# Performance work log

Measured on AMD Instinct MI355X. Metric: run time of the kernel, lower is better.

## Reference

```python
import jax, jax.numpy as jnp
import numpy as np

B, S, I, W, H = 32, 2048, 32, 20, 128  # batch, seq_len, input_size, window_size, hidden_size
LN_EPS = 1e-5


def setup_inputs() -> dict:
    key = jax.random.key(0)
    ks = jax.random.split(key, 12)
    sc = lambda fan: 1.0 / np.sqrt(fan)
    x = jax.random.normal(ks[0], (B, S, I), jnp.float32)
    # encoder: Linear(W*I -> H) + LayerNorm(H) (+ GELU, dropout inactive at eval)
    W_enc = jax.random.normal(ks[1], (W * I, H), jnp.float32) * sc(W * I)
    b_enc = jnp.zeros((H,), jnp.float32)
    gamma = jnp.ones((H,), jnp.float32)
    beta = jnp.zeros((H,), jnp.float32)
    # comparator: Linear(2H->H), GELU, Linear(H->H//2), GELU, Linear(H//2->1), Sigmoid
    W1 = jax.random.normal(ks[2], (2 * H, H), jnp.float32) * sc(2 * H)
    b1 = jnp.zeros((H,), jnp.float32)
    W2 = jax.random.normal(ks[3], (H, H // 2), jnp.float32) * sc(H)
    b2 = jnp.zeros((H // 2,), jnp.float32)
    W3 = jax.random.normal(ks[4], (H // 2, 1), jnp.float32) * sc(H // 2)
    b3 = jnp.zeros((1,), jnp.float32)
    return dict(x=x, W_enc=W_enc, b_enc=b_enc, gamma=gamma, beta=beta,
                W1=W1, b1=b1, W2=W2, b2=b2, W3=W3, b3=b3)


def _gelu(v):
    return jax.nn.gelu(v, approximate=False)  # torch nn.GELU default is exact erf


def reference(x, W_enc, b_enc, gamma, beta, W1, b1, W2, b2, W3, b3):
    Bs, Ss, Is = x.shape
    Wd = W_enc.shape[0] // Is  # window_size
    nwin = Ss - Wd + 1
    # gather all sliding windows once: (B, nwin, Wd*I)
    idx = jnp.arange(nwin)[:, None] + jnp.arange(Wd)[None, :]
    win = x[:, idx, :].reshape(Bs, nwin, Wd * Is)
    # encoder: one big GEMM over all windows (before(t) == window at t-Wd, after(t) == window at t)
    h = win @ W_enc + b_enc
    mu = jnp.mean(h, axis=-1, keepdims=True)
    var = jnp.mean((h - mu) ** 2, axis=-1, keepdims=True)
    enc = _gelu((h - mu) / jnp.sqrt(var + LN_EPS) * gamma + beta)  # (B, nwin, H)
    T = Ss - 2 * Wd  # number of valid changepoint positions t in [Wd, Ss-Wd)
    combined = jnp.concatenate([enc[:, :T], enc[:, Wd:Wd + T]], axis=-1)  # (B, T, 2H)
    z = _gelu(combined @ W1 + b1)
    z = _gelu(z @ W2 + b2)
    p = jax.nn.sigmoid((z @ W3 + b3)[..., 0])  # (B, T)
    probs = jnp.pad(p, ((0, 0), (Wd, Wd)))  # zero pad to (B, S)
    return probs, probs > 0.5
```

## Files before the change

kernel.cpp:

```cpp
#include <hip/hip_runtime.h>
#include <hip/hip_bf16.h>
#include <math.h>

namespace {

constexpr int kB = 32;
constexpr int kS = 2048;
constexpr int kI = 32;
constexpr int kW = 20;
constexpr int kH = 128;
constexpr int kNwin = kS - kW + 1;
constexpr int kT = kS - 2 * kW;
constexpr float kEps = 1e-5f;
constexpr int FCAP = 4096;
constexpr float kMargin = 1e-3f;

typedef __attribute__((ext_vector_type(8))) short short8;
typedef __attribute__((ext_vector_type(8))) unsigned short ush8;
typedef __attribute__((ext_vector_type(4))) float f32x4;

__device__ __forceinline__ unsigned short f2bf(float f) {
    unsigned u = __builtin_bit_cast(unsigned, f);
    u += 0x7FFFu + ((u >> 16) & 1u);
    return (unsigned short)(u >> 16);
}
__device__ __forceinline__ float bf2f(unsigned short h) {
    unsigned u = ((unsigned)h) << 16;
    return __builtin_bit_cast(float, u);
}
__device__ __forceinline__ void split2(float v, unsigned short& hi, unsigned short& lo) {
    hi = f2bf(v);
    lo = f2bf(v - bf2f(hi));
}
__device__ __forceinline__ float gelu_exact(float v) {
    return 0.5f * v * (1.0f + erff(v * 0.70710678118654752440f));
}

constexpr size_t ENCP_OFF = 0;
constexpr size_t WETH_OFF = 33554432;
constexpr size_t WETL_OFF = WETH_OFF + 163840;
constexpr size_t W1TH_OFF = WETL_OFF + 163840;
constexpr size_t W1TL_OFF = W1TH_OFF + 65536;
constexpr size_t W2TH_OFF = W1TL_OFF + 65536;
constexpr size_t W2TL_OFF = W2TH_OFF + 16384;
constexpr size_t FC_OFF   = W2TL_OFF + 16384;
constexpr size_t FL_OFF   = FC_OFF + 64;

__global__ void prep_kernel(const float* __restrict__ Wenc, const float* __restrict__ W1,
                            const float* __restrict__ W2,
                            unsigned short* __restrict__ WeTh, unsigned short* __restrict__ WeTl,
                            unsigned short* __restrict__ W1Th, unsigned short* __restrict__ W1Tl,
                            unsigned short* __restrict__ W2Th, unsigned short* __restrict__ W2Tl)
{
    const int tid = blockIdx.x * blockDim.x + threadIdx.x;
    const int nth = gridDim.x * blockDim.x;
    for (int i = tid; i < kH * 640; i += nth) {
        int n = i / 640, k = i - n * 640;
        split2(Wenc[(size_t)k * kH + n], WeTh[i], WeTl[i]);
    }
    for (int i = tid; i < kH * 256; i += nth) {
        int n = i >> 8, k = i & 255;
        split2(W1[(size_t)k * kH + n], W1Th[i], W1Tl[i]);
    }
    for (int i = tid; i < 64 * kH; i += nth) {
        int n = i >> 7, k = i & 127;
        split2(W2[(size_t)k * 64 + n], W2Th[i], W2Tl[i]);
    }
}

constexpr int AP = 40;

__global__ __launch_bounds__(256, 2)
void enc_kernel(const float* __restrict__ x,
                const unsigned short* __restrict__ WeTh, const unsigned short* __restrict__ WeTl,
                const float* __restrict__ benc, const float* __restrict__ gma,
                const float* __restrict__ bta, unsigned* __restrict__ encp)
{
    __shared__ unsigned short xsh[148 * AP];
    __shared__ unsigned short xsl[148 * AP];
    __shared__ unsigned short wth[2 * 128 * AP];
    __shared__ unsigned short wtl[2 * 128 * AP];

    const int tid = threadIdx.x, b = blockIdx.y, t0 = blockIdx.x * 128;
    const int l = tid & 63, w = tid >> 6;
    const int cb = l & 15, rg = l >> 4;

    const float4* x4 = reinterpret_cast<const float4*>(x + (size_t)b * kS * kI);
    for (int i = tid; i < 148 * 8; i += 256) {
        int r = i >> 3, q = i & 7;
        int gr = t0 + r; if (gr > kS - 1) gr = kS - 1;
        float4 v = x4[gr * 8 + q];
        unsigned short h0, h1, h2, h3, l0, l1, l2, l3;
        split2(v.x, h0, l0); split2(v.y, h1, l1); split2(v.z, h2, l2); split2(v.w, h3, l3);
        *reinterpret_cast<uint2*>(&xsh[r * AP + q * 4]) =
            make_uint2((unsigned)h0 | ((unsigned)h1 << 16), (unsigned)h2 | ((unsigned)h3 << 16));
        *reinterpret_cast<uint2*>(&xsl[r * AP + q * 4]) =
            make_uint2((unsigned)l0 | ((unsigned)l1 << 16), (unsigned)l2 | ((unsigned)l3 << 16));
    }

    f32x4 acc[2][8];
    #pragma unroll
    for (int mi = 0; mi < 2; ++mi)
        #pragma unroll
        for (int nf = 0; nf < 8; ++nf) acc[mi][nf] = f32x4{0.f, 0.f, 0.f, 0.f};

    for (int kc = 0; kc < 10; ++kc) {
        __syncthreads();
        #pragma unroll
        for (int u = 0; u < 4; ++u) {
            int i = tid + 256 * u;
            int n = i >> 3, rem = i & 7;
            int ks = rem >> 2, q = rem & 3;
            size_t so = (size_t)n * 640 + kc * 64 + ks * 32 + q * 8;
            int dd = ks * 128 * AP + n * AP + q * 8;
            *reinterpret_cast<ush8*>(&wth[dd]) = *reinterpret_cast<const ush8*>(WeTh + so);
            *reinterpret_cast<ush8*>(&wtl[dd]) = *reinterpret_cast<const ush8*>(WeTl + so);
        }
        __syncthreads();
        #pragma unroll
        for (int ks = 0; ks < 2; ++ks) {
            const int a0o = (w * 32 + cb + kc * 2 + ks) * AP + rg * 8;
            short8 a0h = *reinterpret_cast<const short8*>(&xsh[a0o]);
            short8 a0l = *reinterpret_cast<const short8*>(&xsl[a0o]);
            short8 a1h = *reinterpret_cast<const short8*>(&xsh[a0o + 16 * AP]);
            short8 a1l = *reinterpret_cast<const short8*>(&xsl[a0o + 16 * AP]);
            #pragma unroll
            for (int nf = 0; nf < 8; ++nf) {
                const int bo = ks * 128 * AP + (nf * 16 + cb) * AP + rg * 8;
                short8 bh = *reinterpret_cast<const short8*>(&wth[bo]);
                short8 bl = *reinterpret_cast<const short8*>(&wtl[bo]);
                acc[0][nf] = __builtin_amdgcn_mfma_f32_16x16x32_bf16(a0h, bh, acc[0][nf], 0, 0, 0);
                acc[0][nf] = __builtin_amdgcn_mfma_f32_16x16x32_bf16(a0l, bh, acc[0][nf], 0, 0, 0);
                acc[0][nf] = __builtin_amdgcn_mfma_f32_16x16x32_bf16(a0h, bl, acc[0][nf], 0, 0, 0);
                acc[1][nf] = __builtin_amdgcn_mfma_f32_16x16x32_bf16(a1h, bh, acc[1][nf], 0, 0, 0);
                acc[1][nf] = __builtin_amdgcn_mfma_f32_16x16x32_bf16(a1l, bh, acc[1][nf], 0, 0, 0);
                acc[1][nf] = __builtin_amdgcn_mfma_f32_16x16x32_bf16(a1h, bl, acc[1][nf], 0, 0, 0);
            }
        }
    }

    float bv[8], gv[8], btv[8];
    #pragma unroll
    for (int nf = 0; nf < 8; ++nf) {
        bv[nf]  = benc[nf * 16 + cb];
        gv[nf]  = gma[nf * 16 + cb];
        btv[nf] = bta[nf * 16 + cb];
    }
    #pragma unroll
    for (int mi = 0; mi < 2; ++mi) {
        #pragma unroll
        for (int r = 0; r < 4; ++r) {
            const int rl = w * 32 + mi * 16 + rg * 4 + r;
            const int t = t0 + rl;
            float h[8];
            float s = 0.f;
            #pragma unroll
            for (int nf = 0; nf < 8; ++nf) { h[nf] = acc[mi][nf][r] + bv[nf]; s += h[nf]; }
            s += __shfl_xor(s, 1); s += __shfl_xor(s, 2); s += __shfl_xor(s, 4); s += __shfl_xor(s, 8);
            const float mu = s * (1.f / 128.f);
            float s2 = 0.f;
            #pragma unroll
            for (int nf = 0; nf < 8; ++nf) { h[nf] -= mu; s2 += h[nf] * h[nf]; }
            s2 += __shfl_xor(s2, 1); s2 += __shfl_xor(s2, 2); s2 += __shfl_xor(s2, 4); s2 += __shfl_xor(s2, 8);
            const float rstd = 1.f / sqrtf(s2 * (1.f / 128.f) + kEps);
            if (t < kNwin) {
                unsigned* dst = encp + ((size_t)(b * kS + t)) * kH;
                #pragma unroll
                for (int nf = 0; nf < 8; ++nf) {
                    float v = gelu_exact(h[nf] * rstd * gv[nf] + btv[nf]);
                    unsigned short hi, lo;
                    split2(v, hi, lo);
                    dst[nf * 16 + cb] = (unsigned)hi | ((unsigned)lo << 16);
                }
            }
        }
    }
}

constexpr int EPP = 72;

__global__ __launch_bounds__(256, 2)
void cmp_kernel(const unsigned* __restrict__ encp,
                const unsigned short* __restrict__ W1Th, const unsigned short* __restrict__ W1Tl,
                const float* __restrict__ b1,
                const unsigned short* __restrict__ W2Th, const unsigned short* __restrict__ W2Tl,
                const float* __restrict__ b2, const float* __restrict__ W3,
                const float* __restrict__ b3, float* __restrict__ out,
                int* __restrict__ fcnt, unsigned* __restrict__ flist)
{
    __shared__ __align__(16) unsigned short pool[29696];
    __shared__ float prm[192];

    unsigned short* esh  = pool;
    unsigned short* esl  = pool + 4608;
    unsigned short* wt1h = pool + 9216;
    unsigned short* wt1l = pool + 19456;

    const int tid = threadIdx.x, b = blockIdx.y, t0 = blockIdx.x * 64;
    const int l = tid & 63, w = tid >> 6;
    const int cb = l & 15, rg = l >> 4;

    if (tid < 128) prm[tid] = b1[tid];
    else if (tid < 192) prm[tid] = b2[tid - 128];

    f32x4 acc1[8];
    #pragma unroll
    for (int nf = 0; nf < 8; ++nf) acc1[nf] = f32x4{0.f, 0.f, 0.f, 0.f};

    for (int kc = 0; kc < 4; ++kc) {
        const int ro = (kc < 2) ? 0 : kW, co = (kc & 1) * 64;
        __syncthreads();
        {
            const int r = tid >> 2, q = tid & 3;
            int gr = t0 + ro + r; if (gr > kNwin - 1) gr = kNwin - 1;
            const unsigned* src = encp + ((size_t)(b * kS + gr)) * kH + co + q * 16;
            #pragma unroll
            for (int j = 0; j < 4; ++j) {
                const uint4 v = *reinterpret_cast<const uint4*>(src + j * 4);
                *reinterpret_cast<uint2*>(&esh[r * EPP + q * 16 + j * 4]) =
                    make_uint2((v.x & 0xFFFFu) | ((v.y & 0xFFFFu) << 16),
                               (v.z & 0xFFFFu) | ((v.w & 0xFFFFu) << 16));
                *reinterpret_cast<uint2*>(&esl[r * EPP + q * 16 + j * 4]) =
                    make_uint2((v.x >> 16) | (v.y & 0xFFFF0000u),
                               (v.z >> 16) | (v.w & 0xFFFF0000u));
            }
        }
        #pragma unroll
        for (int u = 0; u < 4; ++u) {
            int i = tid + 256 * u;
            int n = i >> 3, rem = i & 7;
            int ks = rem >> 2, q = rem & 3;
            size_t so = (size_t)n * 256 + kc * 64 + ks * 32 + q * 8;
            int dd = ks * 128 * AP + n * AP + q * 8;
            *reinterpret_cast<ush8*>(&wt1h[dd]) = *reinterpret_cast<const ush8*>(W1Th + so);
            *reinterpret_cast<ush8*>(&wt1l[dd]) = *reinterpret_cast<const ush8*>(W1Tl + so);
        }
        __syncthreads();
        #pragma unroll
        for (int ks = 0; ks < 2; ++ks) {
            const int ao = (w * 16 + cb) * EPP + ks * 32 + rg * 8;
            short8 ah = *reinterpret_cast<const short8*>(&esh[ao]);
            short8 al = *reinterpret_cast<const short8*>(&esl[ao]);
            #pragma unroll
            for (int nf = 0; nf < 8; ++nf) {
                const int bo = ks * 128 * AP + (nf * 16 + cb) * AP + rg * 8;
                short8 bh = *reinterpret_cast<const short8*>(&wt1h[bo]);
                short8 bl = *reinterpret_cast<const short8*>(&wt1l[bo]);
                acc1[nf] = __builtin_amdgcn_mfma_f32_16x16x32_bf16(ah, bh, acc1[nf], 0, 0, 0);
                acc1[nf] = __builtin_amdgcn_mfma_f32_16x16x32_bf16(al, bh, acc1[nf], 0, 0, 0);
                acc1[nf] = __builtin_amdgcn_mfma_f32_16x16x32_bf16(ah, bl, acc1[nf], 0, 0, 0);
            }
        }
    }
    __syncthreads();
    unsigned short* z1h = pool;
    unsigned short* z1l = pool + 8704;
    unsigned short* w2h = pool + 17408;
    unsigned short* w2l = pool + 22528;
    #pragma unroll
    for (int r = 0; r < 4; ++r) {
        const int row = w * 16 + rg * 4 + r;
        #pragma unroll
        for (int nf = 0; nf < 8; ++nf) {
            float v = gelu_exact(acc1[nf][r] + prm[nf * 16 + cb]);
            unsigned short hi, lo;
            split2(v, hi, lo);
            z1h[row * 136 + nf * 16 + cb] = hi;
            z1l[row * 136 + nf * 16 + cb] = lo;
        }
    }

    f32x4 acc2[4];
    #pragma unroll
    for (int nf = 0; nf < 4; ++nf) acc2[nf] = f32x4{0.f, 0.f, 0.f, 0.f};

    for (int kc = 0; kc < 2; ++kc) {
        __syncthreads();
        #pragma unroll
        for (int u = 0; u < 2; ++u) {
            int i = tid + 256 * u;
            int n = i >> 3, rem = i & 7;
            int ks = rem >> 2, q = rem & 3;
            size_t so = (size_t)n * 128 + kc * 64 + ks * 32 + q * 8;
            int dd = ks * 64 * AP + n * AP + q * 8;
            *reinterpret_cast<ush8*>(&w2h[dd]) = *reinterpret_cast<const ush8*>(W2Th + so);
            *reinterpret_cast<ush8*>(&w2l[dd]) = *reinterpret_cast<const ush8*>(W2Tl + so);
        }
        __syncthreads();
        #pragma unroll
        for (int ks = 0; ks < 2; ++ks) {
            const int ao = (w * 16 + cb) * 136 + kc * 64 + ks * 32 + rg * 8;
            short8 ah = *reinterpret_cast<const short8*>(&z1h[ao]);
            short8 al = *reinterpret_cast<const short8*>(&z1l[ao]);
            #pragma unroll
            for (int nf = 0; nf < 4; ++nf) {
                const int bo = ks * 64 * AP + (nf * 16 + cb) * AP + rg * 8;
                short8 bh = *reinterpret_cast<const short8*>(&w2h[bo]);
                short8 bl = *reinterpret_cast<const short8*>(&w2l[bo]);
                acc2[nf] = __builtin_amdgcn_mfma_f32_16x16x32_bf16(ah, bh, acc2[nf], 0, 0, 0);
                acc2[nf] = __builtin_amdgcn_mfma_f32_16x16x32_bf16(al, bh, acc2[nf], 0, 0, 0);
                acc2[nf] = __builtin_amdgcn_mfma_f32_16x16x32_bf16(ah, bl, acc2[nf], 0, 0, 0);
            }
        }
    }
    __syncthreads();
    float* z2f = reinterpret_cast<float*>(pool);
    #pragma unroll
    for (int r = 0; r < 4; ++r) {
        const int row = w * 16 + rg * 4 + r;
        #pragma unroll
        for (int nf = 0; nf < 4; ++nf)
            z2f[row * 68 + nf * 16 + cb] = gelu_exact(acc2[nf][r] + prm[128 + nf * 16 + cb]);
    }
    __syncthreads();

    if (tid < 64) {
        const int t = t0 + tid;
        if (t < kT) {
            float s = 0.f;
            #pragma unroll 8
            for (int k = 0; k < 64; ++k) s = fmaf(z2f[tid * 68 + k], W3[k], s);
            const float p = 1.f / (1.f + expf(-(s + b3[0])));
            out[(size_t)b * kS + t + kW] = p;
            out[(size_t)kB * kS + (size_t)b * kS + t + kW] = (p > 0.5f) ? 1.f : 0.f;
            if (fabsf(p - 0.5f) < kMargin) {
                int idx = atomicAdd(fcnt, 1);
                if (idx < FCAP) flist[idx] = ((unsigned)b << 16) | (unsigned)t;
            }
        }
    }
}

__global__ __launch_bounds__(256, 4)
void fix2_kernel(const float* __restrict__ x, const float* __restrict__ Wenc,
                 const float* __restrict__ benc, const float* __restrict__ gma,
                 const float* __restrict__ bta, const float* __restrict__ W1,
                 const float* __restrict__ b1, const float* __restrict__ W2,
                 const float* __restrict__ b2, const float* __restrict__ W3,
                 const float* __restrict__ b3, const int* __restrict__ fcnt,
                 const unsigned* __restrict__ flist, float* __restrict__ out)
{
    __shared__ float xw[1280];
    __shared__ float es[256];
    __shared__ float z1s[128];
    __shared__ float z2s[64];
    __shared__ float wred[4];

    const int tid = threadIdx.x;
    int n = *fcnt; if (n > FCAP) n = FCAP;

    for (int i = blockIdx.x; i < n; i += gridDim.x) {
        const unsigned e = flist[i];
        const int b = (int)(e >> 16), t = (int)(e & 0xFFFF);
        __syncthreads();
        for (int j = tid; j < 320; j += 256) {
            int r = (j >= 160) ? 1 : 0, u = j - r * 160;
            const float4 v = *reinterpret_cast<const float4*>(
                x + ((size_t)b * kS + t + r * kW) * kI + u * 4);
            *reinterpret_cast<float4*>(&xw[r * 640 + u * 4]) = v;
        }
        __syncthreads();
        const int r = tid >> 7, c = tid & 127;
        float h = 0.f;
        const float* xr = &xw[r * 640];
        #pragma unroll 16
        for (int k = 0; k < 640; ++k) h = fmaf(xr[k], Wenc[(size_t)k * kH + c], h);
        h += benc[c];
        float s = h;
        #pragma unroll
        for (int m = 1; m < 64; m <<= 1) s += __shfl_xor(s, m, 64);
        if ((tid & 63) == 0) wred[tid >> 6] = s;
        __syncthreads();
        const float mu = (wred[r * 2] + wred[r * 2 + 1]) * (1.f / 128.f);
        const float d = h - mu;
        float s2 = d * d;
        #pragma unroll
        for (int m = 1; m < 64; m <<= 1) s2 += __shfl_xor(s2, m, 64);
        __syncthreads();
        if ((tid & 63) == 0) wred[tid >> 6] = s2;
        __syncthreads();
        const float var = (wred[r * 2] + wred[r * 2 + 1]) * (1.f / 128.f);
        es[tid] = gelu_exact(d * (1.f / sqrtf(var + kEps)) * gma[c] + bta[c]);
        __syncthreads();
        if (tid < kH) {
            float z = 0.f;
            #pragma unroll 16
            for (int k = 0; k < 256; ++k) z = fmaf(es[k], W1[(size_t)k * kH + tid], z);
            z1s[tid] = gelu_exact(z + b1[tid]);
        }
        __syncthreads();
        if (tid < 64) {
            float z = 0.f;
            #pragma unroll 16
            for (int k = 0; k < kH; ++k) z = fmaf(z1s[k], W2[(size_t)k * 64 + tid], z);
            z2s[tid] = gelu_exact(z + b2[tid]);
        }
        __syncthreads();
        if (tid < 64) {
            float s3 = z2s[tid] * W3[tid];
            #pragma unroll
            for (int m = 1; m < 64; m <<= 1) s3 += __shfl_xor(s3, m, 64);
            if (tid == 0) {
                const float p = 1.f / (1.f + expf(-(s3 + b3[0])));
                out[(size_t)b * kS + t + kW] = p;
                out[(size_t)kB * kS + (size_t)b * kS + t + kW] = (p > 0.5f) ? 1.f : 0.f;
            }
        }
        __syncthreads();
    }
}

}

extern "C" void kernel_launch(void* const* d_in, const int* in_sizes, int n_in,
                              void* d_out, int out_size, void* d_ws, size_t ws_size,
                              hipStream_t stream)
{
    const float* x    = (const float*)d_in[0];
    const float* Wenc = (const float*)d_in[1];
    const float* benc = (const float*)d_in[2];
    const float* gma  = (const float*)d_in[3];
    const float* bta  = (const float*)d_in[4];
    const float* W1   = (const float*)d_in[5];
    const float* b1   = (const float*)d_in[6];
    const float* W2   = (const float*)d_in[7];
    const float* b2   = (const float*)d_in[8];
    const float* W3   = (const float*)d_in[9];
    const float* b3   = (const float*)d_in[10];
    float* out = (float*)d_out;

    char* ws = (char*)d_ws;
    unsigned* encp        = (unsigned*)(ws + ENCP_OFF);
    unsigned short* WeTh  = (unsigned short*)(ws + WETH_OFF);
    unsigned short* WeTl  = (unsigned short*)(ws + WETL_OFF);
    unsigned short* W1Th  = (unsigned short*)(ws + W1TH_OFF);
    unsigned short* W1Tl  = (unsigned short*)(ws + W1TL_OFF);
    unsigned short* W2Th  = (unsigned short*)(ws + W2TH_OFF);
    unsigned short* W2Tl  = (unsigned short*)(ws + W2TL_OFF);
    int* fcnt             = (int*)(ws + FC_OFF);
    unsigned* flist       = (unsigned*)(ws + FL_OFF);

    hipMemsetAsync(d_out, 0, (size_t)out_size * sizeof(float), stream);
    hipMemsetAsync(fcnt, 0, 64, stream);

    prep_kernel<<<256, 256, 0, stream>>>(Wenc, W1, W2, WeTh, WeTl, W1Th, W1Tl, W2Th, W2Tl);
    enc_kernel<<<dim3(16, kB), 256, 0, stream>>>(x, WeTh, WeTl, benc, gma, bta, encp);
    cmp_kernel<<<dim3(32, kB), 256, 0, stream>>>(encp, W1Th, W1Tl, b1, W2Th, W2Tl, b2,
                                                 W3, b3, out, fcnt, flist);
    fix2_kernel<<<4096, 256, 0, stream>>>(x, Wenc, benc, gma, bta, W1, b1, W2, b2, W3, b3,
                                          fcnt, flist, out);
}
```

Measured before the change: 137.3 us.

## Split enc and cmp GEMM columns across two waves with 512-thread blocks

New measurement: 132.4 us. -3.5%, faster.

```diff
diff --git a/kernel.cpp b/kernel.cpp
--- a/kernel.cpp
+++ b/kernel.cpp
@@ -70,23 +70,25 @@
 
 constexpr int AP = 40;
 
-__global__ __launch_bounds__(256, 2)
+__global__ __launch_bounds__(512, 4)
 void enc_kernel(const float* __restrict__ x,
                 const unsigned short* __restrict__ WeTh, const unsigned short* __restrict__ WeTl,
                 const float* __restrict__ benc, const float* __restrict__ gma,
                 const float* __restrict__ bta, unsigned* __restrict__ encp)
 {
-    __shared__ unsigned short xsh[148 * AP];
-    __shared__ unsigned short xsl[148 * AP];
-    __shared__ unsigned short wth[2 * 128 * AP];
-    __shared__ unsigned short wtl[2 * 128 * AP];
+    __shared__ unsigned short xsh[147 * AP];
+    __shared__ unsigned short xsl[147 * AP];
+    __shared__ unsigned short wth[128 * AP];
+    __shared__ unsigned short wtl[128 * AP];
+    __shared__ float red[2][128][2];
 
     const int tid = threadIdx.x, b = blockIdx.y, t0 = blockIdx.x * 128;
     const int l = tid & 63, w = tid >> 6;
+    const int wr = w >> 1, wc = w & 1;
     const int cb = l & 15, rg = l >> 4;
 
     const float4* x4 = reinterpret_cast<const float4*>(x + (size_t)b * kS * kI);
-    for (int i = tid; i < 148 * 8; i += 256) {
+    for (int i = tid; i < 147 * 8; i += 512) {
         int r = i >> 3, q = i & 7;
         int gr = t0 + r; if (gr > kS - 1) gr = kS - 1;
         float4 v = x4[gr * 8 + q];
@@ -98,88 +100,105 @@
             make_uint2((unsigned)l0 | ((unsigned)l1 << 16), (unsigned)l2 | ((unsigned)l3 << 16));
     }
 
-    f32x4 acc[2][8];
+    f32x4 acc[2][4];
     #pragma unroll
     for (int mi = 0; mi < 2; ++mi)
         #pragma unroll
-        for (int nf = 0; nf < 8; ++nf) acc[mi][nf] = f32x4{0.f, 0.f, 0.f, 0.f};
-
-    for (int kc = 0; kc < 10; ++kc) {
-        __syncthreads();
-        #pragma unroll
-        for (int u = 0; u < 4; ++u) {
-            int i = tid + 256 * u;
-            int n = i >> 3, rem = i & 7;
-            int ks = rem >> 2, q = rem & 3;
-            size_t so = (size_t)n * 640 + kc * 64 + ks * 32 + q * 8;
-            int dd = ks * 128 * AP + n * AP + q * 8;
-            *reinterpret_cast<ush8*>(&wth[dd]) = *reinterpret_cast<const ush8*>(WeTh + so);
-            *reinterpret_cast<ush8*>(&wtl[dd]) = *reinterpret_cast<const ush8*>(WeTl + so);
-        }
-        __syncthreads();
-        #pragma unroll
-        for (int ks = 0; ks < 2; ++ks) {
-            const int a0o = (w * 32 + cb + kc * 2 + ks) * AP + rg * 8;
-            short8 a0h = *reinterpret_cast<const short8*>(&xsh[a0o]);
-            short8 a0l = *reinterpret_cast<const short8*>(&xsl[a0o]);
-            short8 a1h = *reinterpret_cast<const short8*>(&xsh[a0o + 16 * AP]);
-            short8 a1l = *reinterpret_cast<const short8*>(&xsl[a0o + 16 * AP]);
-            #pragma unroll
-            for (int nf = 0; nf < 8; ++nf) {
-                const int bo = ks * 128 * AP + (nf * 16 + cb) * AP + rg * 8;
-                short8 bh = *reinterpret_cast<const short8*>(&wth[bo]);
-                short8 bl = *reinterpret_cast<const short8*>(&wtl[bo]);
-                acc[0][nf] = __builtin_amdgcn_mfma_f32_16x16x32_bf16(a0h, bh, acc[0][nf], 0, 0, 0);
-                acc[0][nf] = __builtin_amdgcn_mfma_f32_16x16x32_bf16(a0l, bh, acc[0][nf], 0, 0, 0);
-                acc[0][nf] = __builtin_amdgcn_mfma_f32_16x16x32_bf16(a0h, bl, acc[0][nf], 0, 0, 0);
-                acc[1][nf] = __builtin_amdgcn_mfma_f32_16x16x32_bf16(a1h, bh, acc[1][nf], 0, 0, 0);
-                acc[1][nf] = __builtin_amdgcn_mfma_f32_16x16x32_bf16(a1l, bh, acc[1][nf], 0, 0, 0);
-                acc[1][nf] = __builtin_amdgcn_mfma_f32_16x16x32_bf16(a1h, bl, acc[1][nf], 0, 0, 0);
-            }
-        }
-    }
-
-    float bv[8], gv[8], btv[8];
-    #pragma unroll
-    for (int nf = 0; nf < 8; ++nf) {
-        bv[nf]  = benc[nf * 16 + cb];
-        gv[nf]  = gma[nf * 16 + cb];
-        btv[nf] = bta[nf * 16 + cb];
-    }
-    #pragma unroll
-    for (int mi = 0; mi < 2; ++mi) {
+        for (int nf = 0; nf < 4; ++nf) acc[mi][nf] = f32x4{0.f, 0.f, 0.f, 0.f};
+
+    for (int kc = 0; kc < 20; ++kc) {
+        __syncthreads();
+        {
+            const int n = tid >> 2, q = tid & 3;
+            const size_t so = (size_t)n * 640 + kc * 32 + q * 8;
+            *reinterpret_cast<ush8*>(&wth[n * AP + q * 8]) =
+                *reinterpret_cast<const ush8*>(WeTh + so);
+            *reinterpret_cast<ush8*>(&wtl[n * AP + q * 8]) =
+                *reinterpret_cast<const ush8*>(WeTl + so);
+        }
+        __syncthreads();
+        const int a0o = (wr * 32 + cb + kc) * AP + rg * 8;
+        short8 a0h = *reinterpret_cast<const short8*>(&xsh[a0o]);
+        short8 a0l = *reinterpret_cast<const short8*>(&xsl[a0o]);
+        short8 a1h = *reinterpret_cast<const short8*>(&xsh[a0o + 16 * AP]);
+        short8 a1l = *reinterpret_cast<const short8*>(&xsl[a0o + 16 * AP]);
+        #pragma unroll
+        for (int nf = 0; nf < 4; ++nf) {
+            const int bo = (wc * 64 + nf * 16 + cb) * AP + rg * 8;
+            short8 bh = *reinterpret_cast<const short8*>(&wth[bo]);
+            short8 bl = *reinterpret_cast<const short8*>(&wtl[bo]);
+            acc[0][nf] = __builtin_amdgcn_mfma_f32_16x16x32_bf16(a0h, bh, acc[0][nf], 0, 0, 0);
+            acc[0][nf] = __builtin_amdgcn_mfma_f32_16x16x32_bf16(a0l, bh, acc[0][nf], 0, 0, 0);
+            acc[0][nf] = __builtin_amdgcn_mfma_f32_16x16x32_bf16(a0h, bl, acc[0][nf], 0, 0, 0);
+            acc[1][nf] = __builtin_amdgcn_mfma_f32_16x16x32_bf16(a1h, bh, acc[1][nf], 0, 0, 0);
+            acc[1][nf] = __builtin_amdgcn_mfma_f32_16x16x32_bf16(a1l, bh, acc[1][nf], 0, 0, 0);
+            acc[1][nf] = __builtin_amdgcn_mfma_f32_16x16x32_bf16(a1h, bl, acc[1][nf], 0, 0, 0);
+        }
+    }
+
+    float bv[4], gv[4], btv[4];
+    #pragma unroll
+    for (int nf = 0; nf < 4; ++nf) {
+        const int col = wc * 64 + nf * 16 + cb;
+        bv[nf] = benc[col]; gv[nf] = gma[col]; btv[nf] = bta[col];
+    }
+    float h[2][4][4];
+    #pragma unroll
+    for (int mi = 0; mi < 2; ++mi)
         #pragma unroll
         for (int r = 0; r < 4; ++r) {
-            const int rl = w * 32 + mi * 16 + rg * 4 + r;
-            const int t = t0 + rl;
-            float h[8];
             float s = 0.f;
             #pragma unroll
-            for (int nf = 0; nf < 8; ++nf) { h[nf] = acc[mi][nf][r] + bv[nf]; s += h[nf]; }
-            s += __shfl_xor(s, 1); s += __shfl_xor(s, 2); s += __shfl_xor(s, 4); s += __shfl_xor(s, 8);
-            const float mu = s * (1.f / 128.f);
+            for (int nf = 0; nf < 4; ++nf) {
+                h[mi][r][nf] = acc[mi][nf][r] + bv[nf];
+                s += h[mi][r][nf];
+            }
+            s += __shfl_xor(s, 1); s += __shfl_xor(s, 2);
+            s += __shfl_xor(s, 4); s += __shfl_xor(s, 8);
+            if (cb == 0) red[0][wr * 32 + mi * 16 + rg * 4 + r][wc] = s;
+        }
+    __syncthreads();
+    #pragma unroll
+    for (int mi = 0; mi < 2; ++mi)
+        #pragma unroll
+        for (int r = 0; r < 4; ++r) {
+            const int rl = wr * 32 + mi * 16 + rg * 4 + r;
+            const float mu = (red[0][rl][0] + red[0][rl][1]) * (1.f / 128.f);
             float s2 = 0.f;
             #pragma unroll
-            for (int nf = 0; nf < 8; ++nf) { h[nf] -= mu; s2 += h[nf] * h[nf]; }
-            s2 += __shfl_xor(s2, 1); s2 += __shfl_xor(s2, 2); s2 += __shfl_xor(s2, 4); s2 += __shfl_xor(s2, 8);
-            const float rstd = 1.f / sqrtf(s2 * (1.f / 128.f) + kEps);
+            for (int nf = 0; nf < 4; ++nf) {
+                h[mi][r][nf] -= mu;
+                s2 += h[mi][r][nf] * h[mi][r][nf];
+            }
+            s2 += __shfl_xor(s2, 1); s2 += __shfl_xor(s2, 2);
+            s2 += __shfl_xor(s2, 4); s2 += __shfl_xor(s2, 8);
+            if (cb == 0) red[1][rl][wc] = s2;
+        }
+    __syncthreads();
+    #pragma unroll
+    for (int mi = 0; mi < 2; ++mi)
+        #pragma unroll
+        for (int r = 0; r < 4; ++r) {
+            const int rl = wr * 32 + mi * 16 + rg * 4 + r;
+            const int t = t0 + rl;
+            const float var = (red[1][rl][0] + red[1][rl][1]) * (1.f / 128.f);
+            const float rstd = 1.f / sqrtf(var + kEps);
             if (t < kNwin) {
                 unsigned* dst = encp + ((size_t)(b * kS + t)) * kH;
                 #pragma unroll
-                for (int nf = 0; nf < 8; ++nf) {
-                    float v = gelu_exact(h[nf] * rstd * gv[nf] + btv[nf]);
+                for (int nf = 0; nf < 4; ++nf) {
+                    float v = gelu_exact(h[mi][r][nf] * rstd * gv[nf] + btv[nf]);
                     unsigned short hi, lo;
                     split2(v, hi, lo);
-                    dst[nf * 16 + cb] = (unsigned)hi | ((unsigned)lo << 16);
+                    dst[wc * 64 + nf * 16 + cb] = (unsigned)hi | ((unsigned)lo << 16);
                 }
             }
         }
-    }
 }
 
 constexpr int EPP = 72;
 
-__global__ __launch_bounds__(256, 2)
+__global__ __launch_bounds__(512, 4)
 void cmp_kernel(const unsigned* __restrict__ encp,
                 const unsigned short* __restrict__ W1Th, const unsigned short* __restrict__ W1Tl,
                 const float* __restrict__ b1,
@@ -198,36 +217,41 @@
 
     const int tid = threadIdx.x, b = blockIdx.y, t0 = blockIdx.x * 64;
     const int l = tid & 63, w = tid >> 6;
+    const int wr = w >> 1, wc = w & 1;
     const int cb = l & 15, rg = l >> 4;
 
     if (tid < 128) prm[tid] = b1[tid];
     else if (tid < 192) prm[tid] = b2[tid - 128];
 
-    f32x4 acc1[8];
-    #pragma unroll
-    for (int nf = 0; nf < 8; ++nf) acc1[nf] = f32x4{0.f, 0.f, 0.f, 0.f};
+    f32x4 acc1[4];
+    #pragma unroll
+    for (int nf = 0; nf < 4; ++nf) acc1[nf] = f32x4{0.f, 0.f, 0.f, 0.f};
 
     for (int kc = 0; kc < 4; ++kc) {
         const int ro = (kc < 2) ? 0 : kW, co = (kc & 1) * 64;
         __syncthreads();
         {
-            const int r = tid >> 2, q = tid & 3;
+            const int r = tid >> 3, qq = tid & 7;
             int gr = t0 + ro + r; if (gr > kNwin - 1) gr = kNwin - 1;
-            const unsigned* src = encp + ((size_t)(b * kS + gr)) * kH + co + q * 16;
-            #pragma unroll
-            for (int j = 0; j < 4; ++j) {
-                const uint4 v = *reinterpret_cast<const uint4*>(src + j * 4);
-                *reinterpret_cast<uint2*>(&esh[r * EPP + q * 16 + j * 4]) =
-                    make_uint2((v.x & 0xFFFFu) | ((v.y & 0xFFFFu) << 16),
-                               (v.z & 0xFFFFu) | ((v.w & 0xFFFFu) << 16));
-                *reinterpret_cast<uint2*>(&esl[r * EPP + q * 16 + j * 4]) =
-                    make_uint2((v.x >> 16) | (v.y & 0xFFFF0000u),
-                               (v.z >> 16) | (v.w & 0xFFFF0000u));
-            }
-        }
-        #pragma unroll
-        for (int u = 0; u < 4; ++u) {
-            int i = tid + 256 * u;
+            const unsigned* src = encp + ((size_t)(b * kS + gr)) * kH + co + qq * 8;
+            const uint4 v0 = *reinterpret_cast<const uint4*>(src);
+            const uint4 v1 = *reinterpret_cast<const uint4*>(src + 4);
+            *reinterpret_cast<uint2*>(&esh[r * EPP + qq * 8]) =
+                make_uint2((v0.x & 0xFFFFu) | ((v0.y & 0xFFFFu) << 16),
+                           (v0.z & 0xFFFFu) | ((v0.w & 0xFFFFu) << 16));
+            *reinterpret_cast<uint2*>(&esh[r * EPP + qq * 8 + 4]) =
+                make_uint2((v1.x & 0xFFFFu) | ((v1.y & 0xFFFFu) << 16),
+                           (v1.z & 0xFFFFu) | ((v1.w & 0xFFFFu) << 16));
+            *reinterpret_cast<uint2*>(&esl[r * EPP + qq * 8]) =
+                make_uint2((v0.x >> 16) | (v0.y & 0xFFFF0000u),
+                           (v0.z >> 16) | (v0.w & 0xFFFF0000u));
+            *reinterpret_cast<uint2*>(&esl[r * EPP + qq * 8 + 4]) =
+                make_uint2((v1.x >> 16) | (v1.y & 0xFFFF0000u),
+                           (v1.z >> 16) | (v1.w & 0xFFFF0000u));
+        }
+        #pragma unroll
+        for (int u = 0; u < 2; ++u) {
+            int i = tid + 512 * u;
             int n = i >> 3, rem = i & 7;
             int ks = rem >> 2, q = rem & 3;
             size_t so = (size_t)n * 256 + kc * 64 + ks * 32 + q * 8;
@@ -238,12 +262,12 @@
         __syncthreads();
         #pragma unroll
         for (int ks = 0; ks < 2; ++ks) {
-            const int ao = (w * 16 + cb) * EPP + ks * 32 + rg * 8;
+            const int ao = (wr * 16 + cb) * EPP + ks * 32 + rg * 8;
             short8 ah = *reinterpret_cast<const short8*>(&esh[ao]);
             short8 al = *reinterpret_cast<const short8*>(&esl[ao]);
             #pragma unroll
-            for (int nf = 0; nf < 8; ++nf) {
-                const int bo = ks * 128 * AP + (nf * 16 + cb) * AP + rg * 8;
+            for (int nf = 0; nf < 4; ++nf) {
+                const int bo = ks * 128 * AP + (wc * 64 + nf * 16 + cb) * AP + rg * 8;
                 short8 bh = *reinterpret_cast<const short8*>(&wt1h[bo]);
                 short8 bl = *reinterpret_cast<const short8*>(&wt1l[bo]);
                 acc1[nf] = __builtin_amdgcn_mfma_f32_16x16x32_bf16(ah, bh, acc1[nf], 0, 0, 0);
@@ -259,42 +283,41 @@
     unsigned short* w2l = pool + 22528;
     #pragma unroll
     for (int r = 0; r < 4; ++r) {
-        const int row = w * 16 + rg * 4 + r;
-        #pragma unroll
-        for (int nf = 0; nf < 8; ++nf) {
-            float v = gelu_exact(acc1[nf][r] + prm[nf * 16 + cb]);
+        const int row = wr * 16 + rg * 4 + r;
+        #pragma unroll
+        for (int nf = 0; nf < 4; ++nf) {
+            const int col = wc * 64 + nf * 16 + cb;
+            float v = gelu_exact(acc1[nf][r] + prm[col]);
             unsigned short hi, lo;
             split2(v, hi, lo);
-            z1h[row * 136 + nf * 16 + cb] = hi;
-            z1l[row * 136 + nf * 16 + cb] = lo;
-        }
-    }
-
-    f32x4 acc2[4];
-    #pragma unroll
-    for (int nf = 0; nf < 4; ++nf) acc2[nf] = f32x4{0.f, 0.f, 0.f, 0.f};
-
-    for (int kc = 0; kc < 2; ++kc) {
-        __syncthreads();
-        #pragma unroll
-        for (int u = 0; u < 2; ++u) {
-            int i = tid + 256 * u;
-            int n = i >> 3, rem = i & 7;
-            int ks = rem >> 2, q = rem & 3;
-            size_t so = (size_t)n * 128 + kc * 64 + ks * 32 + q * 8;
-            int dd = ks * 64 * AP + n * AP + q * 8;
+            z1h[row * 136 + col] = hi;
+            z1l[row * 136 + col] = lo;
+        }
+    }
+
+    f32x4 acc2[2];
+    #pragma unroll
+    for (int nf = 0; nf < 2; ++nf) acc2[nf] = f32x4{0.f, 0.f, 0.f, 0.f};
+
+    for (int kc2 = 0; kc2 < 2; ++kc2) {
+        __syncthreads();
+        {
+            const int n = tid >> 3, rem = tid & 7;
+            const int ks = rem >> 2, q = rem & 3;
+            const size_t so = (size_t)n * 128 + kc2 * 64 + ks * 32 + q * 8;
+            const int dd = ks * 64 * AP + n * AP + q * 8;
             *reinterpret_cast<ush8*>(&w2h[dd]) = *reinterpret_cast<const ush8*>(W2Th + so);
             *reinterpret_cast<ush8*>(&w2l[dd]) = *reinterpret_cast<const ush8*>(W2Tl + so);
         }
         __syncthreads();
         #pragma unroll
         for (int ks = 0; ks < 2; ++ks) {
-            const int ao = (w * 16 + cb) * 136 + kc * 64 + ks * 32 + rg * 8;
+            const int ao = (wr * 16 + cb) * 136 + kc2 * 64 + ks * 32 + rg * 8;
             short8 ah = *reinterpret_cast<const short8*>(&z1h[ao]);
             short8 al = *reinterpret_cast<const short8*>(&z1l[ao]);
             #pragma unroll
-            for (int nf = 0; nf < 4; ++nf) {
-                const int bo = ks * 64 * AP + (nf * 16 + cb) * AP + rg * 8;
+            for (int nf = 0; nf < 2; ++nf) {
+                const int bo = ks * 64 * AP + (wc * 32 + nf * 16 + cb) * AP + rg * 8;
                 short8 bh = *reinterpret_cast<const short8*>(&w2h[bo]);
                 short8 bl = *reinterpret_cast<const short8*>(&w2l[bo]);
                 acc2[nf] = __builtin_amdgcn_mfma_f32_16x16x32_bf16(ah, bh, acc2[nf], 0, 0, 0);
@@ -307,10 +330,12 @@
     float* z2f = reinterpret_cast<float*>(pool);
     #pragma unroll
     for (int r = 0; r < 4; ++r) {
-        const int row = w * 16 + rg * 4 + r;
-        #pragma unroll
-        for (int nf = 0; nf < 4; ++nf)
-            z2f[row * 68 + nf * 16 + cb] = gelu_exact(acc2[nf][r] + prm[128 + nf * 16 + cb]);
+        const int row = wr * 16 + rg * 4 + r;
+        #pragma unroll
+        for (int nf = 0; nf < 2; ++nf) {
+            const int col = wc * 32 + nf * 16 + cb;
+            z2f[row * 68 + col] = gelu_exact(acc2[nf][r] + prm[128 + col]);
+        }
     }
     __syncthreads();
 
@@ -444,8 +469,8 @@
     hipMemsetAsync(fcnt, 0, 64, stream);
 
     prep_kernel<<<256, 256, 0, stream>>>(Wenc, W1, W2, WeTh, WeTl, W1Th, W1Tl, W2Th, W2Tl);
-    enc_kernel<<<dim3(16, kB), 256, 0, stream>>>(x, WeTh, WeTl, benc, gma, bta, encp);
-    cmp_kernel<<<dim3(32, kB), 256, 0, stream>>>(encp, W1Th, W1Tl, b1, W2Th, W2Tl, b2,
+    enc_kernel<<<dim3(16, kB), 512, 0, stream>>>(x, WeTh, WeTl, benc, gma, bta, encp);
+    cmp_kernel<<<dim3(32, kB), 512, 0, stream>>>(encp, W1Th, W1Tl, b1, W2Th, W2Tl, b2,
                                                  W3, b3, out, fcnt, flist);
     fix2_kernel<<<4096, 256, 0, stream>>>(x, Wenc, benc, gma, bta, W1, b1, W2, b2, W3, b3,
                                           fcnt, flist, out);
```
